# Performance work log

Measured on AMD Instinct MI355X. Metric: run time of the kernel, lower is better.

## Reference

```python
import jax, jax.numpy as jnp
import numpy as np

N, T, U, D, V = 8, 200, 100, 512, 500


def setup_inputs() -> dict:
    key = jax.random.key(0)
    k1, k2, k3, k4 = jax.random.split(key, 4)
    encoder_out = jax.random.normal(k1, (N, T, D), dtype=jnp.float32)
    decoder_out = jax.random.normal(k2, (N, U, D), dtype=jnp.float32)
    # nn.Linear(input_dim, output_dim): weight (V, D), bias (V,)
    bound = 1.0 / np.sqrt(D)
    W = jax.random.uniform(k3, (V, D), minval=-bound, maxval=bound, dtype=jnp.float32)
    b = jax.random.uniform(k4, (V,), minval=-bound, maxval=bound, dtype=jnp.float32)
    return {"encoder_out": encoder_out, "decoder_out": decoder_out, "W": W, "b": b}


def reference(encoder_out, decoder_out, W, b):
    # broadcast add: (N,T,1,D) + (N,1,U,D) -> (N,T,U,D)
    x = encoder_out[:, :, None, :] + decoder_out[:, None, :, :]
    activations = jnp.tanh(x)
    # linear: (N,T,U,D) @ (D,V) + b -> (N,T,U,V)
    logits = jnp.einsum("ntud,vd->ntuv", activations, W) + b
    return logits
```

## Files before the change

### kernel.cpp

```cpp
#include <hip/hip_runtime.h>
#include <hip/hip_bf16.h>


#define NB 8
#define TT 200
#define UU 100
#define DD 512
#define VV 500
#define VP 512
#define BM 64
#define BNB 256
#define BK 32
#define KSTEPS 16
#define THREADS 256
#define LDA 40
#define LCH 264
#define MROWS (NB*TT*UU)
#define MBLOCKS (MROWS/BM)

typedef __attribute__((ext_vector_type(4))) float  f32x4;
typedef __attribute__((ext_vector_type(8))) short  s16x8;

__device__ __forceinline__ unsigned short f2bf(float f) {
    unsigned int u = __builtin_bit_cast(unsigned int, f);
    u = (u + 0x7FFFu + ((u >> 16) & 1u)) >> 16;
    return (unsigned short)u;
}

__device__ __forceinline__ float fast_tanh(float x) {
    float e = __expf(2.0f * x);
    return 1.0f - 2.0f * __builtin_amdgcn_rcpf(e + 1.0f);
}

__global__ void prep_w(const float* __restrict__ W, unsigned short* __restrict__ Wt) {
    int idx = blockIdx.x * 256 + threadIdx.x;
    int k = idx & 511;
    int v = idx >> 9;
    float val = (v < VV) ? W[v * DD + k] : 0.0f;
    Wt[(k >> 5) * (VP * BK) + v * BK + (k & 31)] = f2bf(val);
}

__global__ __launch_bounds__(THREADS, 3) void joiner_kernel(
    const float* __restrict__ enc, const float* __restrict__ dec,
    const unsigned short* __restrict__ Wt, const float* __restrict__ bias,
    float* __restrict__ out)
{
    __shared__ __align__(16) char smem[16 * LCH * 4];
    unsigned short* lA0 = (unsigned short*)smem;
    unsigned short* lA1 = (unsigned short*)(smem + BM * LDA * 2);

    const int tid  = threadIdx.x;
    const int mb   = blockIdx.x;
    const int vb   = blockIdx.y;
    const int lane = tid & 63;
    const int wn   = tid >> 6;
    const int lr   = lane & 15;
    const int lk   = lane >> 4;

    const int srow = tid >> 2;
    const int sk   = (tid & 3) << 3;

    int r   = mb * BM + srow;
    int n   = r / (TT * UU);
    int rem = r - n * (TT * UU);
    int t   = rem / UU;
    int u   = rem - t * UU;
    const float* ep = enc + (n * TT + t) * DD + sk;
    const float* dp = dec + (n * UU + u) * DD + sk;

    f32x4 e0, e1, d0, d1;

    e0 = *(const f32x4*)(ep);     e1 = *(const f32x4*)(ep + 4);
    d0 = *(const f32x4*)(dp);     d1 = *(const f32x4*)(dp + 4);
    {
        s16x8 av;
        #pragma unroll
        for (int j = 0; j < 4; ++j) av[j]     = (short)f2bf(fast_tanh(e0[j] + d0[j]));
        #pragma unroll
        for (int j = 0; j < 4; ++j) av[4 + j] = (short)f2bf(fast_tanh(e1[j] + d1[j]));
        *(s16x8*)(&lA0[srow * LDA + sk]) = av;
    }
    e0 = *(const f32x4*)(ep + BK);     e1 = *(const f32x4*)(ep + BK + 4);
    d0 = *(const f32x4*)(dp + BK);     d1 = *(const f32x4*)(dp + BK + 4);
    __syncthreads();

    f32x4 acc[4][4];
    #pragma unroll
    for (int m = 0; m < 4; ++m)
        #pragma unroll
        for (int f = 0; f < 4; ++f)
            acc[m][f] = (f32x4){0.f, 0.f, 0.f, 0.f};

    const unsigned short* wptr = Wt + (vb * BNB + wn * 64 + lr) * BK + lk * 8;

    for (int kc = 0; kc < KSTEPS; ++kc) {
        unsigned short* lCur = (kc & 1) ? lA1 : lA0;
        unsigned short* lNxt = (kc & 1) ? lA0 : lA1;

        s16x8 bF[4];
        #pragma unroll
        for (int f = 0; f < 4; ++f)
            bF[f] = *(const s16x8*)(wptr + kc * (VP * BK) + f * (16 * BK));

        s16x8 aF[4];
        #pragma unroll
        for (int m = 0; m < 4; ++m)
            aF[m] = *(const s16x8*)(&lCur[(m * 16 + lr) * LDA + lk * 8]);

        if (kc < KSTEPS - 1) {
            s16x8 av;
            #pragma unroll
            for (int j = 0; j < 4; ++j) av[j]     = (short)f2bf(fast_tanh(e0[j] + d0[j]));
            #pragma unroll
            for (int j = 0; j < 4; ++j) av[4 + j] = (short)f2bf(fast_tanh(e1[j] + d1[j]));
            *(s16x8*)(&lNxt[srow * LDA + sk]) = av;
            if (kc < KSTEPS - 2) {
                const float* ep2 = ep + (kc + 2) * BK;
                const float* dp2 = dp + (kc + 2) * BK;
                e0 = *(const f32x4*)(ep2);     e1 = *(const f32x4*)(ep2 + 4);
                d0 = *(const f32x4*)(dp2);     d1 = *(const f32x4*)(dp2 + 4);
            }
        }

        __builtin_amdgcn_s_setprio(1);
        #pragma unroll
        for (int m = 0; m < 4; ++m)
            #pragma unroll
            for (int f = 0; f < 4; ++f)
                acc[m][f] = __builtin_amdgcn_mfma_f32_16x16x32_bf16(aF[m], bF[f], acc[m][f], 0, 0, 0);
        __builtin_amdgcn_s_setprio(0);

        __syncthreads();
    }

    float bv[4];
    #pragma unroll
    for (int f = 0; f < 4; ++f) {
        int v = vb * BNB + wn * 64 + f * 16 + lr;
        bv[f] = (v < VV) ? bias[v] : 0.0f;
    }

    float* lchunk = (float*)smem;
    const int slabcols = (vb == 0) ? BNB : (VV - BNB);
    const int segmax   = slabcols >> 2;
    float* outbase = out + (long)mb * BM * VV + vb * BNB;

    for (int c = 0; c < 4; ++c) {
        __syncthreads();
        #pragma unroll
        for (int f = 0; f < 4; ++f) {
            int vloc = wn * 64 + f * 16 + lr;
            #pragma unroll
            for (int q = 0; q < 4; ++q)
                lchunk[(lk * 4 + q) * LCH + vloc] = acc[c][f][q] + bv[f];
        }
        __syncthreads();
        float* dst = outbase + c * 16 * VV;
        #pragma unroll
        for (int i = 0; i < 4; ++i) {
            int idx = i * THREADS + tid;
            int row = idx >> 6;
            int seg = idx & 63;
            if (seg < segmax)
                *(f32x4*)(dst + row * VV + seg * 4) =
                    *(const f32x4*)(lchunk + row * LCH + seg * 4);
        }
    }
}

extern "C" void kernel_launch(void* const* d_in, const int* in_sizes, int n_in,
                              void* d_out, int out_size, void* d_ws, size_t ws_size,
                              hipStream_t stream) {
    const float* enc = (const float*)d_in[0];
    const float* dec = (const float*)d_in[1];
    const float* W   = (const float*)d_in[2];
    const float* b   = (const float*)d_in[3];
    float* out = (float*)d_out;
    unsigned short* Wt = (unsigned short*)d_ws;

    prep_w<<<dim3((VP * DD) / 256), dim3(256), 0, stream>>>(W, Wt);
    joiner_kernel<<<dim3(MBLOCKS, 2), dim3(THREADS), 0, stream>>>(enc, dec, Wt, b, out);
}
```

Before: 157.3 us.

## Software-pipeline W fragment loads and defer tanh after MFMAs with packed bf16 convert

New measurement: 154.0 us. -2.1%, faster.

```diff
diff --git a/kernel.cpp b/kernel.cpp
--- a/kernel.cpp
+++ b/kernel.cpp
@@ -18,8 +18,9 @@
 #define MROWS (NB*TT*UU)
 #define MBLOCKS (MROWS/BM)
 
-typedef __attribute__((ext_vector_type(4))) float  f32x4;
-typedef __attribute__((ext_vector_type(8))) short  s16x8;
+typedef __attribute__((ext_vector_type(4))) float         f32x4;
+typedef __attribute__((ext_vector_type(8))) short         s16x8;
+typedef __attribute__((ext_vector_type(4))) unsigned int  u32x4;
 
 __device__ __forceinline__ unsigned short f2bf(float f) {
     unsigned int u = __builtin_bit_cast(unsigned int, f);
@@ -27,9 +28,15 @@
     return (unsigned short)u;
 }
 
+__device__ __forceinline__ unsigned int cvt_pk_bf16(float a, float b) {
+    unsigned int r;
+    asm("v_cvt_pk_bf16_f32 %0, %1, %2" : "=v"(r) : "v"(a), "v"(b));
+    return r;
+}
+
 __device__ __forceinline__ float fast_tanh(float x) {
-    float e = __expf(2.0f * x);
-    return 1.0f - 2.0f * __builtin_amdgcn_rcpf(e + 1.0f);
+    float e = __builtin_amdgcn_exp2f(x * 2.88539008177793f);
+    return __builtin_fmaf(-2.0f, __builtin_amdgcn_rcpf(e + 1.0f), 1.0f);
 }
 
 __global__ void prep_w(const float* __restrict__ W, unsigned short* __restrict__ Wt) {
@@ -39,6 +46,40 @@
     float val = (v < VV) ? W[v * DD + k] : 0.0f;
     Wt[(k >> 5) * (VP * BK) + v * BK + (k & 31)] = f2bf(val);
 }
+
+#define KBODY(kc, CUR, NXT, BC, BNX)                                          \
+  {                                                                           \
+    if ((kc) < KSTEPS - 1) {                                                  \
+      _Pragma("unroll")                                                       \
+      for (int f = 0; f < 4; ++f)                                             \
+        BNX[f] = *(const s16x8*)(wptr + ((kc)+1) * (VP * BK) + f * (16*BK));  \
+      const float* e2 = ep + ((kc)+1) * BK;                                   \
+      const float* d2 = dp + ((kc)+1) * BK;                                   \
+      e0 = *(const f32x4*)(e2);  e1 = *(const f32x4*)(e2 + 4);                \
+      d0 = *(const f32x4*)(d2);  d1 = *(const f32x4*)(d2 + 4);                \
+    }                                                                         \
+    s16x8 aF[4];                                                              \
+    _Pragma("unroll")                                                         \
+    for (int m = 0; m < 4; ++m)                                               \
+      aF[m] = *(const s16x8*)(&CUR[(m * 16 + lr) * LDA + lk * 8]);            \
+    __builtin_amdgcn_s_setprio(1);                                            \
+    _Pragma("unroll")                                                         \
+    for (int m = 0; m < 4; ++m)                                               \
+      _Pragma("unroll")                                                       \
+      for (int f = 0; f < 4; ++f)                                             \
+        acc[m][f] = __builtin_amdgcn_mfma_f32_16x16x32_bf16(aF[m], BC[f],     \
+                                                            acc[m][f],0,0,0); \
+    __builtin_amdgcn_s_setprio(0);                                            \
+    if ((kc) < KSTEPS - 1) {                                                  \
+      u32x4 wds;                                                              \
+      wds[0] = cvt_pk_bf16(fast_tanh(e0[0]+d0[0]), fast_tanh(e0[1]+d0[1]));   \
+      wds[1] = cvt_pk_bf16(fast_tanh(e0[2]+d0[2]), fast_tanh(e0[3]+d0[3]));   \
+      wds[2] = cvt_pk_bf16(fast_tanh(e1[0]+d1[0]), fast_tanh(e1[1]+d1[1]));   \
+      wds[3] = cvt_pk_bf16(fast_tanh(e1[2]+d1[2]), fast_tanh(e1[3]+d1[3]));   \
+      *(u32x4*)(&NXT[srow * LDA + sk]) = wds;                                 \
+    }                                                                         \
+    __syncthreads();                                                          \
+  }
 
 __global__ __launch_bounds__(THREADS, 3) void joiner_kernel(
     const float* __restrict__ enc, const float* __restrict__ dec,
@@ -68,20 +109,24 @@
     const float* ep = enc + (n * TT + t) * DD + sk;
     const float* dp = dec + (n * UU + u) * DD + sk;
 
+    const unsigned short* wptr = Wt + (vb * BNB + wn * 64 + lr) * BK + lk * 8;
+
     f32x4 e0, e1, d0, d1;
+    s16x8 b0[4], b1[4];
 
     e0 = *(const f32x4*)(ep);     e1 = *(const f32x4*)(ep + 4);
     d0 = *(const f32x4*)(dp);     d1 = *(const f32x4*)(dp + 4);
+    #pragma unroll
+    for (int f = 0; f < 4; ++f)
+        b0[f] = *(const s16x8*)(wptr + f * (16 * BK));
     {
-        s16x8 av;
-        #pragma unroll
-        for (int j = 0; j < 4; ++j) av[j]     = (short)f2bf(fast_tanh(e0[j] + d0[j]));
-        #pragma unroll
-        for (int j = 0; j < 4; ++j) av[4 + j] = (short)f2bf(fast_tanh(e1[j] + d1[j]));
-        *(s16x8*)(&lA0[srow * LDA + sk]) = av;
+        u32x4 wds;
+        wds[0] = cvt_pk_bf16(fast_tanh(e0[0]+d0[0]), fast_tanh(e0[1]+d0[1]));
+        wds[1] = cvt_pk_bf16(fast_tanh(e0[2]+d0[2]), fast_tanh(e0[3]+d0[3]));
+        wds[2] = cvt_pk_bf16(fast_tanh(e1[0]+d1[0]), fast_tanh(e1[1]+d1[1]));
+        wds[3] = cvt_pk_bf16(fast_tanh(e1[2]+d1[2]), fast_tanh(e1[3]+d1[3]));
+        *(u32x4*)(&lA0[srow * LDA + sk]) = wds;
     }
-    e0 = *(const f32x4*)(ep + BK);     e1 = *(const f32x4*)(ep + BK + 4);
-    d0 = *(const f32x4*)(dp + BK);     d1 = *(const f32x4*)(dp + BK + 4);
     __syncthreads();
 
     f32x4 acc[4][4];
@@ -91,46 +136,10 @@
         for (int f = 0; f < 4; ++f)
             acc[m][f] = (f32x4){0.f, 0.f, 0.f, 0.f};
 
-    const unsigned short* wptr = Wt + (vb * BNB + wn * 64 + lr) * BK + lk * 8;
-
-    for (int kc = 0; kc < KSTEPS; ++kc) {
-        unsigned short* lCur = (kc & 1) ? lA1 : lA0;
-        unsigned short* lNxt = (kc & 1) ? lA0 : lA1;
-
-        s16x8 bF[4];
-        #pragma unroll
-        for (int f = 0; f < 4; ++f)
-            bF[f] = *(const s16x8*)(wptr + kc * (VP * BK) + f * (16 * BK));
-
-        s16x8 aF[4];
-        #pragma unroll
-        for (int m = 0; m < 4; ++m)
-            aF[m] = *(const s16x8*)(&lCur[(m * 16 + lr) * LDA + lk * 8]);
-
-        if (kc < KSTEPS - 1) {
-            s16x8 av;
-            #pragma unroll
-            for (int j = 0; j < 4; ++j) av[j]     = (short)f2bf(fast_tanh(e0[j] + d0[j]));
-            #pragma unroll
-            for (int j = 0; j < 4; ++j) av[4 + j] = (short)f2bf(fast_tanh(e1[j] + d1[j]));
-            *(s16x8*)(&lNxt[srow * LDA + sk]) = av;
-            if (kc < KSTEPS - 2) {
-                const float* ep2 = ep + (kc + 2) * BK;
-                const float* dp2 = dp + (kc + 2) * BK;
-                e0 = *(const f32x4*)(ep2);     e1 = *(const f32x4*)(ep2 + 4);
-                d0 = *(const f32x4*)(dp2);     d1 = *(const f32x4*)(dp2 + 4);
-            }
-        }
-
-        __builtin_amdgcn_s_setprio(1);
-        #pragma unroll
-        for (int m = 0; m < 4; ++m)
-            #pragma unroll
-            for (int f = 0; f < 4; ++f)
-                acc[m][f] = __builtin_amdgcn_mfma_f32_16x16x32_bf16(aF[m], bF[f], acc[m][f], 0, 0, 0);
-        __builtin_amdgcn_s_setprio(0);
-
-        __syncthreads();
+    #pragma unroll
+    for (int kk = 0; kk < KSTEPS; kk += 2) {
+        KBODY(kk,     lA0, lA1, b0, b1)
+        KBODY(kk + 1, lA1, lA0, b1, b0)
     }
 
     float bv[4];
```
